# Performance work log

Hardware: AMD Instinct MI355X
Metric: run time of the kernel (lower is better)

## Reference

```python
import jax, jax.numpy as jnp
import numpy as np

N_NODES = 8192
N_EDGES = 262144
N_PATHS = 1000000
MAX_PATH = 5
EDGE_DIM = 32


def setup_inputs() -> dict:
    key = jax.random.key(0)
    k1, k2, k3, k4, k5, k6, k7 = jax.random.split(key, 7)
    return {
        "x": jax.random.normal(k1, (N_NODES, EDGE_DIM), dtype=jnp.float32),
        "edge_attr": jax.random.normal(k2, (N_EDGES, EDGE_DIM), dtype=jnp.float32),
        "edge_weights": jax.random.normal(k3, (MAX_PATH, EDGE_DIM), dtype=jnp.float32),
        "paths": jax.random.randint(k4, (N_PATHS, MAX_PATH), 0, N_EDGES, dtype=jnp.int64),
        "path_lens": jax.random.randint(k5, (N_PATHS,), 0, MAX_PATH + 1, dtype=jnp.int64),
        "src": jax.random.randint(k6, (N_PATHS,), 0, N_NODES, dtype=jnp.int64),
        "dst": jax.random.randint(k7, (N_PATHS,), 0, N_NODES, dtype=jnp.int64),
    }


def reference(x, edge_attr, edge_weights, paths, path_lens, src, dst):
    # Per-path gather of edge features: [P, L, D]
    feats = edge_attr[paths]
    # Per-hop dot product with the learned per-hop weight vector: [P, L]
    hop_dots = jnp.einsum("pld,ld->pl", feats, edge_weights)
    # Mask hops beyond each path's length (original slices path[:len]).
    L = edge_weights.shape[0]
    hop_mask = jnp.arange(L)[None, :] < path_lens[:, None]  # [P, L]
    s = jnp.sum(jnp.where(hop_mask, hop_dots, 0.0), axis=1)  # [P]
    lens_f = path_lens.astype(s.dtype)
    # Mean over path hops (zero-length paths -> 0, matching nan_to_num).
    enc = jnp.where(path_lens > 0, s / jnp.maximum(lens_f, 1.0), 0.0)
    n = x.shape[0]
    cij = jnp.zeros((n, n), dtype=x.dtype).at[src, dst].set(enc)
    return jnp.nan_to_num(cij)
```

## Files before the change

kernel.cpp:

```cpp
#include <hip/hip_runtime.h>

#define N_NODES_C 8192
#define MAX_PATH_C 5
#define EDGE_DIM_C 32

__global__ void __launch_bounds__(256) ee_pass1_winner(
    const int* __restrict__ src, const int* __restrict__ dst,
    unsigned int* __restrict__ outw, int P)
{
    int p = blockIdx.x * blockDim.x + threadIdx.x;
    if (p >= P) return;
    long long cell = (long long)src[p] * N_NODES_C + (long long)dst[p];
    atomicMax(outw + cell, (unsigned int)(p + 1));
}

__global__ void __launch_bounds__(256) ee_pass2_enc(
    const float* __restrict__ edge_attr,
    const float* __restrict__ edge_weights,
    const int* __restrict__ paths,
    const int* __restrict__ path_lens,
    const int* __restrict__ src, const int* __restrict__ dst,
    float* __restrict__ out, int P)
{
    __shared__ __align__(16) float w[MAX_PATH_C * EDGE_DIM_C];
    for (int i = threadIdx.x; i < MAX_PATH_C * EDGE_DIM_C; i += blockDim.x)
        w[i] = edge_weights[i];
    __syncthreads();

    int p = blockIdx.x * blockDim.x + threadIdx.x;
    if (p >= P) return;

    long long cell = (long long)src[p] * N_NODES_C + (long long)dst[p];
    const unsigned int* outw = (const unsigned int*)out;
    if (outw[cell] != (unsigned int)(p + 1)) return;

    int len = (int)path_lens[p];
    float s = 0.0f;
    #pragma unroll
    for (int l = 0; l < MAX_PATH_C; ++l) {
        if (l < len) {
            long long e = (long long)paths[p * MAX_PATH_C + l];
            const float4* __restrict__ row =
                (const float4*)(edge_attr + e * EDGE_DIM_C);
            const float4* wr = (const float4*)(w + l * EDGE_DIM_C);
            float acc = 0.0f;
            #pragma unroll
            for (int j = 0; j < EDGE_DIM_C / 4; ++j) {
                float4 a = row[j];
                float4 b = wr[j];
                acc += a.x * b.x + a.y * b.y + a.z * b.z + a.w * b.w;
            }
            s += acc;
        }
    }
    float enc = (len > 0) ? s / (float)len : 0.0f;
    if (isnan(enc)) enc = 0.0f;
    out[cell] = enc;
}

extern "C" void kernel_launch(void* const* d_in, const int* in_sizes, int n_in,
                              void* d_out, int out_size, void* d_ws, size_t ws_size,
                              hipStream_t stream)
{
    const float* edge_attr    = (const float*)d_in[1];
    const float* edge_weights = (const float*)d_in[2];
    const int*   paths        = (const int*)d_in[3];
    const int*   path_lens    = (const int*)d_in[4];
    const int*   src          = (const int*)d_in[5];
    const int*   dst          = (const int*)d_in[6];
    float* out = (float*)d_out;
    const int P = in_sizes[4];

    hipMemsetAsync(d_out, 0, (size_t)out_size * sizeof(float), stream);

    const int threads = 256;
    const int blocks = (P + threads - 1) / threads;
    ee_pass1_winner<<<blocks, threads, 0, stream>>>(
        src, dst, (unsigned int*)out, P);
    ee_pass2_enc<<<blocks, threads, 0, stream>>>(
        edge_attr, edge_weights, paths, path_lens, src, dst, out, P);
}
```

Measured before the change: 168.0 us.

## Bucket paths by source row and resolve winners in LDS per row

Replaces the global memset plus global atomicMax winner pass with a counting sort of paths by src row (histogram, scan, scatter). A per-row block then resolves the last-writer winner with LDS atomics and writes the full row with nontemporal vector stores. Encodings are now computed for every path rather than only winners. This removes the separate 256MB memset and the random global atomics, at the cost of extra kernels, a single-block scan, and atomic scatter contention on src counters.

```diff
diff --git a/kernel.cpp b/kernel.cpp
--- a/kernel.cpp
+++ b/kernel.cpp
@@ -4,23 +4,28 @@
 #define MAX_PATH_C 5
 #define EDGE_DIM_C 32
 
-__global__ void __launch_bounds__(256) ee_pass1_winner(
-    const int* __restrict__ src, const int* __restrict__ dst,
-    unsigned int* __restrict__ outw, int P)
+typedef unsigned int uint4_v __attribute__((ext_vector_type(4)));
+
+#define WS_CNT    0
+#define WS_OFFS   8192
+#define WS_CURSOR 24576
+#define WS_PATHID 32768
+#define WS_ENC    (32768 + 1048576)
+
+__global__ void __launch_bounds__(256) k_init(unsigned int* __restrict__ cnt)
 {
-    int p = blockIdx.x * blockDim.x + threadIdx.x;
-    if (p >= P) return;
-    long long cell = (long long)src[p] * N_NODES_C + (long long)dst[p];
-    atomicMax(outw + cell, (unsigned int)(p + 1));
+    int i = blockIdx.x * blockDim.x + threadIdx.x;
+    if (i < N_NODES_C) cnt[i] = 0u;
 }
 
-__global__ void __launch_bounds__(256) ee_pass2_enc(
+__global__ void __launch_bounds__(256) k_hist_enc(
     const float* __restrict__ edge_attr,
     const float* __restrict__ edge_weights,
     const int* __restrict__ paths,
     const int* __restrict__ path_lens,
-    const int* __restrict__ src, const int* __restrict__ dst,
-    float* __restrict__ out, int P)
+    const int* __restrict__ src,
+    unsigned int* __restrict__ cnt,
+    float* __restrict__ enc_out, int P)
 {
     __shared__ __align__(16) float w[MAX_PATH_C * EDGE_DIM_C];
     for (int i = threadIdx.x; i < MAX_PATH_C * EDGE_DIM_C; i += blockDim.x)
@@ -30,11 +35,9 @@
     int p = blockIdx.x * blockDim.x + threadIdx.x;
     if (p >= P) return;
 
-    long long cell = (long long)src[p] * N_NODES_C + (long long)dst[p];
-    const unsigned int* outw = (const unsigned int*)out;
-    if (outw[cell] != (unsigned int)(p + 1)) return;
+    atomicAdd(&cnt[src[p]], 1u);
 
-    int len = (int)path_lens[p];
+    int len = path_lens[p];
     float s = 0.0f;
     #pragma unroll
     for (int l = 0; l < MAX_PATH_C; ++l) {
@@ -55,7 +58,84 @@
     }
     float enc = (len > 0) ? s / (float)len : 0.0f;
     if (isnan(enc)) enc = 0.0f;
-    out[cell] = enc;
+    enc_out[p] = enc;
+}
+
+__global__ void __launch_bounds__(1024) k_scan(
+    const unsigned int* __restrict__ cnt,
+    unsigned int* __restrict__ offs,
+    unsigned int* __restrict__ cursor)
+{
+    __shared__ unsigned int part[1024];
+    int t = threadIdx.x;
+    unsigned int local[8];
+    unsigned int mysum = 0;
+    #pragma unroll
+    for (int j = 0; j < 8; ++j) { local[j] = cnt[t * 8 + j]; mysum += local[j]; }
+    part[t] = mysum;
+    __syncthreads();
+    for (int off = 1; off < 1024; off <<= 1) {
+        unsigned int v = 0;
+        if (t >= off) v = part[t - off];
+        __syncthreads();
+        if (t >= off) part[t] += v;
+        __syncthreads();
+    }
+    unsigned int run = part[t] - mysum;
+    #pragma unroll
+    for (int j = 0; j < 8; ++j) {
+        offs[t * 8 + j] = run;
+        cursor[t * 8 + j] = run;
+        run += local[j];
+    }
+    if (t == 1023) offs[N_NODES_C] = run;
+}
+
+__global__ void __launch_bounds__(256) k_scatter(
+    const int* __restrict__ src,
+    unsigned int* __restrict__ cursor,
+    unsigned int* __restrict__ pathid, int P)
+{
+    int p = blockIdx.x * blockDim.x + threadIdx.x;
+    if (p >= P) return;
+    unsigned int pos = atomicAdd(&cursor[src[p]], 1u);
+    pathid[pos] = (unsigned int)p;
+}
+
+__global__ void __launch_bounds__(256) k_sweep(
+    const unsigned int* __restrict__ offs,
+    const unsigned int* __restrict__ pathid,
+    const float* __restrict__ enc,
+    const int* __restrict__ dst,
+    float* __restrict__ out)
+{
+    __shared__ __align__(16) unsigned int row[N_NODES_C];
+    const int r = blockIdx.x;
+    const int t = threadIdx.x;
+
+    uint4_v* row4 = (uint4_v*)row;
+    uint4_v z = (uint4_v)(0u);
+    #pragma unroll
+    for (int j = 0; j < 8; ++j) row4[j * 256 + t] = z;
+    __syncthreads();
+
+    const unsigned int beg = offs[r], end = offs[r + 1];
+    for (unsigned int i = beg + t; i < end; i += 256) {
+        unsigned int p = pathid[i];
+        atomicMax(&row[dst[p]], p + 1u);
+    }
+    __syncthreads();
+    for (unsigned int i = beg + t; i < end; i += 256) {
+        unsigned int p = pathid[i];
+        int d = dst[p];
+        if (row[d] == p + 1u) row[d] = __float_as_uint(enc[p]);
+    }
+    __syncthreads();
+
+    uint4_v* out4 = (uint4_v*)(out + (size_t)r * N_NODES_C);
+    #pragma unroll
+    for (int j = 0; j < 8; ++j)
+        __builtin_nontemporal_store(row4[j * 256 + t], &out4[j * 256 + t]);
 }
 
 extern "C" void kernel_launch(void* const* d_in, const int* in_sizes, int n_in,
@@ -71,12 +151,20 @@
     float* out = (float*)d_out;
     const int P = in_sizes[4];
 
-    hipMemsetAsync(d_out, 0, (size_t)out_size * sizeof(float), stream);
+    unsigned int* ws_u = (unsigned int*)d_ws;
+    unsigned int* cnt    = ws_u + WS_CNT;
+    unsigned int* offs   = ws_u + WS_OFFS;
+    unsigned int* cursor = ws_u + WS_CURSOR;
+    unsigned int* pathid = ws_u + WS_PATHID;
+    float*        enc    = (float*)(ws_u + WS_ENC);
 
     const int threads = 256;
-    const int blocks = (P + threads - 1) / threads;
-    ee_pass1_winner<<<blocks, threads, 0, stream>>>(
-        src, dst, (unsigned int*)out, P);
-    ee_pass2_enc<<<blocks, threads, 0, stream>>>(
-        edge_attr, edge_weights, paths, path_lens, src, dst, out, P);
+    const int pblocks = (P + threads - 1) / threads;
+
+    k_init<<<(N_NODES_C + threads - 1) / threads, threads, 0, stream>>>(cnt);
+    k_hist_enc<<<pblocks, threads, 0, stream>>>(
+        edge_attr, edge_weights, paths, path_lens, src, cnt, enc, P);
+    k_scan<<<1, 1024, 0, stream>>>(cnt, offs, cursor);
+    k_scatter<<<pblocks, threads, 0, stream>>>(src, cursor, pathid, P);
+    k_sweep<<<N_NODES_C, threads, 0, stream>>>(offs, pathid, enc, dst, out);
 }
```

Result: slower. 174.6 us (+3.9%).
